# Kernel optimization log

Measured on AMD Instinct MI355X. Metric: run time of the kernel, lower is better.

## Reference

```python
import jax, jax.numpy as jnp
import numpy as np

N_NODES = 50000
N_EDGES = 800000
D_IN = 128
D_OUT = 128
N_GRAPHS = 64
NEG_SLOPE = 0.01  # torch F.leaky_relu default


def gcn_conv(x, W, b, src, dst, n_nodes):
    """PyG GCNConv: linear, add self-loops, symmetric norm, scatter-add, bias."""
    h = x @ W  # [N, D_OUT]
    # degree including self-loop (edge_weight = 1)
    deg = jnp.zeros((n_nodes,), x.dtype).at[dst].add(1.0) + 1.0
    dinv = jax.lax.rsqrt(deg)
    norm = dinv[src] * dinv[dst]           # [E]
    agg = jnp.zeros_like(h).at[dst].add(h[src] * norm[:, None])
    # self-loop contribution: dinv[i]*dinv[i]*h[i] = h[i]/deg[i]
    return agg + h * (1.0 / deg)[:, None] + b


def gcn_branch(x, edge_index, Ws, bs):
    src, dst = edge_index[0], edge_index[1]
    n = x.shape[0]
    for W, b in zip(Ws, bs):
        x = gcn_conv(x, W, b, src, dst, n)
        x = jax.nn.leaky_relu(x, NEG_SLOPE)
        # dropout is identity in eval mode
    return x


def mean_pool(x, batch, num_graphs):
    s = jax.ops.segment_sum(x, batch, num_segments=num_graphs)
    cnt = jax.ops.segment_sum(jnp.ones((x.shape[0],), x.dtype), batch, num_segments=num_graphs)
    return s / jnp.maximum(cnt, 1.0)[:, None]


def setup_inputs() -> dict:
    key = jax.random.key(0)
    ks = jax.random.split(key, 20)
    inp = {
        'x1': jax.random.normal(ks[0], (N_NODES, D_IN), jnp.float32),
        'edge_index1': jax.random.randint(ks[1], (2, N_EDGES), 0, N_NODES, jnp.int64 if jax.config.jax_enable_x64 else jnp.int32),
        'batch1': jnp.sort(jax.random.randint(ks[2], (N_NODES,), 0, N_GRAPHS)),
        'x2': jax.random.normal(ks[3], (N_NODES, D_IN), jnp.float32),
        'edge_index2': jax.random.randint(ks[4], (2, N_EDGES), 0, N_NODES, jnp.int64 if jax.config.jax_enable_x64 else jnp.int32),
        'batch2': jnp.sort(jax.random.randint(ks[5], (N_NODES,), 0, N_GRAPHS)),
    }
    s = 1.0 / np.sqrt(D_IN)
    inp['W1_0'] = jax.random.uniform(ks[6], (D_IN, D_OUT), jnp.float32, -s, s)
    inp['b1_0'] = jnp.zeros((D_OUT,), jnp.float32)
    inp['W1_1'] = jax.random.uniform(ks[7], (D_OUT, D_OUT), jnp.float32, -s, s)
    inp['b1_1'] = jnp.zeros((D_OUT,), jnp.float32)
    inp['W2_0'] = jax.random.uniform(ks[8], (D_IN, D_OUT), jnp.float32, -s, s)
    inp['b2_0'] = jnp.zeros((D_OUT,), jnp.float32)
    inp['W2_1'] = jax.random.uniform(ks[9], (D_OUT, D_OUT), jnp.float32, -s, s)
    inp['b2_1'] = jnp.zeros((D_OUT,), jnp.float32)
    s2 = 1.0 / np.sqrt(2 * D_OUT)
    inp['lin1_W'] = jax.random.uniform(ks[10], (2 * D_OUT, D_OUT), jnp.float32, -s2, s2)
    inp['lin1_b'] = jax.random.uniform(ks[11], (D_OUT,), jnp.float32, -s2, s2)
    s3 = 1.0 / np.sqrt(D_OUT)
    inp['lin2_W'] = jax.random.uniform(ks[12], (D_OUT, 1), jnp.float32, -s3, s3)
    inp['lin2_b'] = jax.random.uniform(ks[13], (1,), jnp.float32, -s3, s3)
    return inp


def reference(x1, edge_index1, batch1, x2, edge_index2, batch2,
              W1_0, b1_0, W1_1, b1_1, W2_0, b2_0, W2_1, b2_1,
              lin1_W, lin1_b, lin2_W, lin2_b):
    h1 = gcn_branch(x1, edge_index1, [W1_0, W1_1], [b1_0, b1_1])
    h1 = mean_pool(h1, batch1, N_GRAPHS)
    h2 = gcn_branch(x2, edge_index2, [W2_0, W2_1], [b2_0, b2_1])
    h2 = mean_pool(h2, batch2, N_GRAPHS)
    h = jnp.concatenate([h1, h2], axis=-1)  # [G, 256]
    h = jax.nn.relu(h @ lin1_W + lin1_b)
    return h @ lin2_W + lin2_b  # [G, 1]
```

## Files before the change

kernel.cpp:

```cpp
#include <hip/hip_runtime.h>
#include <hip/hip_fp16.h>

#define N_NODES 50000
#define N_EDGES 800000
#define D 128
#define N_GRAPHS 64
#define NEG_SLOPE 0.01f
#define ELLW 32
#define OVF_CAP 8192

#define BUCKETS 196
#define NPAD (BUCKETS * 256)
#define EPB 2048
#define BCAP 5120
#define XS 136
#define NR (N_NODES + 16)
#define EMPTY_IDX 50000
#define EMPTY_FILL 0xC350C350u
#define AGG_BLKS (N_NODES / 16)

typedef _Float16 half8 __attribute__((ext_vector_type(8)));
typedef _Float16 half4 __attribute__((ext_vector_type(4)));
typedef float f32x4 __attribute__((ext_vector_type(4)));
typedef float f32x2 __attribute__((ext_vector_type(2)));

__device__ __forceinline__ int lower_bound_i(const int* __restrict__ arr, int n, int key) {
    int lo = 0, hi = n;
    while (lo < hi) {
        int mid = (lo + hi) >> 1;
        if (arr[mid] < key) lo = mid + 1; else hi = mid;
    }
    return lo;
}

__global__ __launch_bounds__(256) void k_prep(const float* __restrict__ Wa, const float* __restrict__ Wb,
                                              const float* __restrict__ Wc, const float* __restrict__ Wd,
                                              const int* __restrict__ batch1, const int* __restrict__ batch2,
                                              __half* __restrict__ WtH, int* __restrict__ gcnt,
                                              float* __restrict__ pp, int* __restrict__ cntg,
                                              unsigned char* __restrict__ H8a, unsigned char* __restrict__ H8b) {
    const float* Ws[4] = {Wa, Wb, Wc, Wd};
    const float* W = Ws[blockIdx.x];
    __half* o = WtH + (size_t)blockIdx.x * 16384;
    int t = threadIdx.x;
    for (int r = 0; r < 64; r++) {
        int e = r * 256 + t;
        int k = e >> 7, n = e & 127;
        o[n * 128 + k] = __float2half(W[k * 128 + n]);
    }
#pragma unroll
    for (int i = 0; i < 16; i++) pp[blockIdx.x * 4096 + i * 256 + t] = 0.0f;
    {
        unsigned char* z = (blockIdx.x < 2 ? H8a : H8b) + (size_t)(blockIdx.x & 1) * NR * 128 + (size_t)N_NODES * 128;
        if (t < 32) ((unsigned int*)z)[t] = 0u;
    }
    if (blockIdx.x == 0) {
        for (int i = t; i < 2 * BUCKETS + 8; i += 256) gcnt[i] = 0;
    }
    if (blockIdx.x == 1) {
        if (t < 64)
            cntg[t] = lower_bound_i(batch1, N_NODES, t + 1) - lower_bound_i(batch1, N_NODES, t);
        else if (t < 128)
            cntg[t] = lower_bound_i(batch2, N_NODES, (t - 64) + 1) - lower_bound_i(batch2, N_NODES, t - 64);
    }
}

__global__ __launch_bounds__(256) void k_part(const int* __restrict__ ei1, const int* __restrict__ ei2,
                                              int* __restrict__ gcnt, int2* __restrict__ bucketed) {
    const int br = blockIdx.x & 1;
    const int blk = blockIdx.x >> 1;
    const int* __restrict__ src = (br ? ei2 : ei1);
    const int* __restrict__ dst = src + N_EDGES;
    int* __restrict__ gc = gcnt + br * BUCKETS;
    int2* __restrict__ bk = bucketed + (size_t)br * BUCKETS * BCAP;

    __shared__ int bcnt[BUCKETS];
    __shared__ int bofs[BUCKETS];
    __shared__ int gbase[BUCKETS];
    __shared__ int sc[BUCKETS];
    __shared__ int stot;
    __shared__ int2 stage[EPB];
    const int tid = threadIdx.x;
    const int base = blk * EPB;
    for (int b = tid; b < BUCKETS; b += 256) bcnt[b] = 0;
    __syncthreads();
    int d_[8], s_[8], p_[8];
#pragma unroll
    for (int k = 0; k < 8; k++) {
        int i = base + k * 256 + tid;
        bool v = i < N_EDGES;
        d_[k] = v ? dst[i] : -1;
        s_[k] = v ? src[i] : 0;
        p_[k] = 0;
        if (v) p_[k] = atomicAdd(&bcnt[d_[k] >> 8], 1);
    }
    __syncthreads();
    if (tid < BUCKETS) sc[tid] = bcnt[tid];
    __syncthreads();
    for (int off = 1; off < BUCKETS; off <<= 1) {
        int v = (tid < BUCKETS && tid >= off) ? sc[tid - off] : 0;
        __syncthreads();
        if (tid < BUCKETS) sc[tid] += v;
        __syncthreads();
    }
    if (tid < BUCKETS) {
        bofs[tid] = sc[tid] - bcnt[tid];
        gbase[tid] = atomicAdd(&gc[tid], bcnt[tid]);
    }
    if (tid == BUCKETS - 1) stot = sc[tid];
    __syncthreads();
#pragma unroll
    for (int k = 0; k < 8; k++) {
        if (d_[k] >= 0) stage[bofs[d_[k] >> 8] + p_[k]] = make_int2(d_[k], s_[k]);
    }
    __syncthreads();
    int total = stot;
    for (int i = tid; i < total; i += 256) {
        int2 e = stage[i];
        int b = e.x >> 8;
        int dest = gbase[b] + (i - bofs[b]);
        if (dest < BCAP) bk[(size_t)b * BCAP + dest] = e;
    }
}

__global__ __launch_bounds__(256) void k_build(const int* __restrict__ gcnt, const int2* __restrict__ bucketed,
                                               int* __restrict__ cnti, unsigned short* __restrict__ ell,
                                               int2* __restrict__ ovf, int* __restrict__ ocnt) {
    const int br = blockIdx.x & 1;
    const int b = blockIdx.x >> 1;
    const int* __restrict__ gc = gcnt + br * BUCKETS;
    const int2* __restrict__ bk = bucketed + (size_t)br * BUCKETS * BCAP;
    int* __restrict__ ci = cnti + br * NPAD;
    unsigned short* __restrict__ el = ell + (size_t)br * NPAD * ELLW;
    int2* __restrict__ ov = ovf + (size_t)br * OVF_CAP;
    int* __restrict__ oc = ocnt + br;

    __shared__ unsigned short lell[256 * ELLW];
    __shared__ int lcnt[256];
    const int tid = threadIdx.x;
    lcnt[tid] = 0;
#pragma unroll
    for (int i = 0; i < 4; i++) ((uint4*)lell)[tid + 256 * i] = make_uint4(EMPTY_FILL, EMPTY_FILL, EMPTY_FILL, EMPTY_FILL);
    __syncthreads();
    int nb = min(gc[b], BCAP);
    const int2* __restrict__ bp = bk + (size_t)b * BCAP;
    for (int i = tid; i < nb; i += 256) {
        int2 e = bp[i];
        int dl = e.x & 255;
        int p = atomicAdd(&lcnt[dl], 1);
        if (p < ELLW) {
            lell[dl * ELLW + p] = (unsigned short)e.y;
        } else {
            int o = atomicAdd(oc, 1);
            if (o < OVF_CAP) ov[o] = e;
        }
    }
    __syncthreads();
    ci[b * 256 + tid] = lcnt[tid];
    uint4* eg = (uint4*)(el + (size_t)b * 256 * ELLW);
    const uint4* elc = (const uint4*)lell;
    for (int i = tid; i < 256 * ELLW * 2 / 16; i += 256) eg[i] = elc[i];
}

template <bool FP16IN>
__global__ __launch_bounds__(256) void k_gemm(const void* __restrict__ xin1, const void* __restrict__ xin2,
                                              const __half* __restrict__ WtHall, int layer,
                                              const int* __restrict__ cnti, unsigned char* __restrict__ H8) {
    const int br = blockIdx.y;
    const void* __restrict__ xin = (br ? xin2 : xin1);
    const __half* __restrict__ WtH = WtHall + (size_t)(br * 2 + layer) * 16384;
    const int* __restrict__ cnt = cnti + br * NPAD;
    unsigned char* __restrict__ h = H8 + (size_t)br * NR * 128;

    __shared__ _Float16 Xl[64 * XS];
    __shared__ _Float16 Wt[128 * XS];
    const int tid = threadIdx.x;
    const int w = tid >> 6, lane = tid & 63;
    const int quad = lane >> 4, l16 = lane & 15;
    const int row0 = blockIdx.x * 64;

#pragma unroll
    for (int i = 0; i < 8; i++) {
        int i2 = tid + 256 * i;
        int r = i2 >> 4, cg = i2 & 15;
        *(uint4*)&Wt[r * XS + cg * 8] = ((const uint4*)WtH)[i2];
    }
    if (FP16IN) {
        const __half* x = (const __half*)xin;
#pragma unroll
        for (int i = 0; i < 4; i++) {
            int i2 = tid + 256 * i;
            int r = i2 >> 4, cg = i2 & 15;
            uint4 v = make_uint4(0, 0, 0, 0);
            if (row0 + r < N_NODES) v = ((const uint4*)(x + (size_t)(row0 + r) * D))[cg];
            *(uint4*)&Xl[r * XS + cg * 8] = v;
        }
    } else {
        const float* x = (const float*)xin;
#pragma unroll
        for (int i = 0; i < 8; i++) {
            int i2 = tid + 256 * i;
            int r = i2 >> 5, f4 = i2 & 31;
            float4 v = make_float4(0.f, 0.f, 0.f, 0.f);
            if (row0 + r < N_NODES) v = *(const float4*)((const float*)x + (size_t)(row0 + r) * D + f4 * 4);
            half4 hv;
            hv[0] = (_Float16)v.x; hv[1] = (_Float16)v.y; hv[2] = (_Float16)v.z; hv[3] = (_Float16)v.w;
            *(half4*)&Xl[r * XS + f4 * 4] = hv;
        }
    }
    __syncthreads();

    half8 a[4];
#pragma unroll
    for (int kb = 0; kb < 4; kb++)
        a[kb] = *(const half8*)&Xl[(w * 16 + l16) * XS + kb * 32 + quad * 8];

    const int rbase = row0 + w * 16 + quad * 4;
    float di[4];
#pragma unroll
    for (int reg = 0; reg < 4; reg++) {
        int r = rbase + reg;
        di[reg] = (r < N_NODES) ? rsqrtf((float)cnt[r] + 1.0f) : 0.0f;
    }

    float accs[8][4];
#pragma unroll
    for (int ct = 0; ct < 8; ct++) {
        f32x4 acc = {0.f, 0.f, 0.f, 0.f};
#pragma unroll
        for (int kb = 0; kb < 4; kb++) {
            half8 b = *(const half8*)&Wt[(ct * 16 + l16) * XS + kb * 32 + quad * 8];
            acc = __builtin_amdgcn_mfma_f32_16x16x32_f16(a[kb], b, acc, 0, 0, 0);
        }
#pragma unroll
        for (int reg = 0; reg < 4; reg++) accs[ct][reg] = acc[reg] * di[reg];
    }

    __syncthreads();
    unsigned char* S = (unsigned char*)Xl;
#pragma unroll
    for (int ct = 0; ct < 8; ct++)
#pragma unroll
        for (int reg = 0; reg < 4; reg++) {
            int p = __builtin_amdgcn_cvt_pk_fp8_f32(accs[ct][reg], accs[ct][reg], 0, false);
            S[(w * 16 + quad * 4 + reg) * 128 + ct * 16 + l16] = (unsigned char)p;
        }
    __syncthreads();
#pragma unroll
    for (int i = 0; i < 2; i++) {
        int idx = tid + 256 * i;
        int r = idx >> 3, cg = idx & 7;
        if (row0 + r < N_NODES)
            ((uint4*)(h + (size_t)(row0 + r) * 128))[cg] = ((const uint4*)S)[idx];
    }
}

#define AGG_ISSUE(buf, g) do {                                                             \
    unsigned int iw0 = *(const unsigned int*)&sidx[nq][(g) * 8 + 0];                       \
    unsigned int iw1 = *(const unsigned int*)&sidx[nq][(g) * 8 + 2];                       \
    unsigned int iw2 = *(const unsigned int*)&sidx[nq][(g) * 8 + 4];                       \
    unsigned int iw3 = *(const unsigned int*)&sidx[nq][(g) * 8 + 6];                       \
    buf[0] = *(const unsigned int*)(H8 + (size_t)(iw0 & 0xffffu) * 128 + hofs + l16 * 4);  \
    buf[1] = *(const unsigned int*)(H8 + (size_t)(iw0 >> 16) * 128 + hofs + l16 * 4);      \
    buf[2] = *(const unsigned int*)(H8 + (size_t)(iw1 & 0xffffu) * 128 + hofs + l16 * 4);  \
    buf[3] = *(const unsigned int*)(H8 + (size_t)(iw1 >> 16) * 128 + hofs + l16 * 4);      \
    buf[4] = *(const unsigned int*)(H8 + (size_t)(iw2 & 0xffffu) * 128 + hofs + l16 * 4);  \
    buf[5] = *(const unsigned int*)(H8 + (size_t)(iw2 >> 16) * 128 + hofs + l16 * 4);      \
    buf[6] = *(const unsigned int*)(H8 + (size_t)(iw3 & 0xffffu) * 128 + hofs + l16 * 4);  \
    buf[7] = *(const unsigned int*)(H8 + (size_t)(iw3 >> 16) * 128 + hofs + l16 * 4);      \
} while (0)

#define AGG_CONSUME(buf) do {                                                              \
    _Pragma("unroll")                                                                      \
    for (int i_ = 0; i_ < 8; i_++) {                                                       \
        f32x2 lo = __builtin_amdgcn_cvt_pk_f32_fp8((int)buf[i_], false);                   \
        f32x2 hi = __builtin_amdgcn_cvt_pk_f32_fp8((int)buf[i_], true);                    \
        accv[i_ & 3].x += lo[0];                                                           \
        accv[i_ & 3].y += lo[1];                                                           \
        accv[i_ & 3].z += hi[0];                                                           \
        accv[i_ & 3].w += hi[1];                                                           \
    }                                                                                      \
} while (0)

#define AGG_CORE()                                                                         \
    float4 accv[4];                                                                        \
    {                                                                                      \
        f32x2 lo = __builtin_amdgcn_cvt_pk_f32_fp8((int)dself, false);                     \
        f32x2 hi = __builtin_amdgcn_cvt_pk_f32_fp8((int)dself, true);                      \
        accv[0] = make_float4(lo[0], lo[1], hi[0], hi[1]);                                 \
    }                                                                                      \
    accv[1] = make_float4(0.f, 0.f, 0.f, 0.f); accv[2] = accv[1]; accv[3] = accv[1];       \
    unsigned int bA_[8], bB_[8], bC_[8], bD_[8];                                           \
    AGG_ISSUE(bA_, 0);                                                                     \
    if (nc > 8)  { AGG_ISSUE(bB_, 1); }                                                    \
    if (nc > 16) { AGG_ISSUE(bC_, 2); }                                                    \
    if (nc > 24) { AGG_ISSUE(bD_, 3); }                                                    \
    AGG_CONSUME(bA_);                                                                      \
    if (nc > 8)  { AGG_CONSUME(bB_); }                                                     \
    if (nc > 16) { AGG_CONSUME(bC_); }                                                     \
    if (nc > 24) { AGG_CONSUME(bD_); }

__global__ __launch_bounds__(256) void k_agg(const int* __restrict__ cnti, const unsigned short* __restrict__ ell,
                                             const int2* __restrict__ ovf, const int* __restrict__ ocnt,
                                             const unsigned char* __restrict__ H8all, const float* __restrict__ bias1,
                                             const float* __restrict__ bias2, __half* __restrict__ ACT) {
    const int tid = threadIdx.x;
    const int l16 = tid & 15;
    const int nq = tid >> 4;
    const int br = blockIdx.x & 1;
    const int rest = blockIdx.x >> 1;
    const int half = rest >= AGG_BLKS ? 1 : 0;
    const int blk = rest - half * AGG_BLKS;
    const int node = blk * 16 + nq;
    const int hofs = half * 64;

    const int* __restrict__ cnt = cnti + br * NPAD;
    const unsigned short* __restrict__ el = ell + (size_t)br * NPAD * ELLW;
    const int2* __restrict__ ov = ovf + (size_t)br * OVF_CAP;
    const unsigned char* __restrict__ H8 = H8all + (size_t)br * NR * 128;
    const float* __restrict__ bias = (br ? bias2 : bias1);
    __half* __restrict__ out = ACT + (size_t)br * N_NODES * D;

    __shared__ unsigned short sidx[16][ELLW];
    if (tid < 64) ((uint4*)sidx)[tid] = ((const uint4*)(el + (size_t)blk * 16 * ELLW))[tid];

    int n = cnt[node];
    int nc = min(n, ELLW);
    unsigned int dself = *(const unsigned int*)(H8 + (size_t)node * 128 + hofs + l16 * 4);
    __syncthreads();

    AGG_CORE();

    if (n > ELLW) {
        int oc = min(ocnt[br], OVF_CAP);
        for (int o = 0; o < oc; o++) {
            int2 p = ov[o];
            if (p.x == node) {
                unsigned int dw = *(const unsigned int*)(H8 + (size_t)p.y * 128 + hofs + l16 * 4);
                f32x2 lo = __builtin_amdgcn_cvt_pk_f32_fp8((int)dw, false);
                f32x2 hi = __builtin_amdgcn_cvt_pk_f32_fp8((int)dw, true);
                accv[0].x += lo[0]; accv[0].y += lo[1]; accv[0].z += hi[0]; accv[0].w += hi[1];
            }
        }
    }
    float sx = (accv[0].x + accv[1].x) + (accv[2].x + accv[3].x);
    float sy = (accv[0].y + accv[1].y) + (accv[2].y + accv[3].y);
    float sz = (accv[0].z + accv[1].z) + (accv[2].z + accv[3].z);
    float sw = (accv[0].w + accv[1].w) + (accv[2].w + accv[3].w);
    float dv = rsqrtf((float)n + 1.0f);
    float4 b = ((const float4*)bias)[half * 16 + l16];
    float vx = sx * dv + b.x;
    float vy = sy * dv + b.y;
    float vz = sz * dv + b.z;
    float vw = sw * dv + b.w;
    vx = vx > 0.0f ? vx : NEG_SLOPE * vx;
    vy = vy > 0.0f ? vy : NEG_SLOPE * vy;
    vz = vz > 0.0f ? vz : NEG_SLOPE * vz;
    vw = vw > 0.0f ? vw : NEG_SLOPE * vw;
    union { __half2 h2[2]; uint2 u; } up;
    up.h2[0] = __floats2half2_rn(vx, vy);
    up.h2[1] = __floats2half2_rn(vz, vw);
    *(uint2*)(out + (size_t)node * 128 + half * 64 + l16 * 4) = up.u;
}

__global__ __launch_bounds__(256) void k_aggpool(const int* __restrict__ cnti, const unsigned short* __restrict__ ell,
                                                 const int2* __restrict__ ovf, const int* __restrict__ ocnt,
                                                 const unsigned char* __restrict__ H8all,
                                                 const float* __restrict__ bias1, const float* __restrict__ bias2,
                                                 const int* __restrict__ batch1, const int* __restrict__ batch2,
                                                 float* __restrict__ ppall) {
    const int tid = threadIdx.x;
    const int l16 = tid & 15;
    const int nq = tid >> 4;
    const int br = blockIdx.x & 1;
    const int rest = blockIdx.x >> 1;
    const int half = rest >= AGG_BLKS ? 1 : 0;
    const int blk = rest - half * AGG_BLKS;
    const int node = blk * 16 + nq;
    const int hofs = half * 64;

    const int* __restrict__ cnt = cnti + br * NPAD;
    const unsigned short* __restrict__ el = ell + (size_t)br * NPAD * ELLW;
    const int2* __restrict__ ov = ovf + (size_t)br * OVF_CAP;
    const unsigned char* __restrict__ H8 = H8all + (size_t)br * NR * 128;
    const float* __restrict__ bias = (br ? bias2 : bias1);
    const int* __restrict__ batch = (br ? batch2 : batch1);
    float* __restrict__ pp = ppall + (size_t)br * N_GRAPHS * D;

    __shared__ unsigned short sidx[16][ELLW];
    if (tid < 64) ((uint4*)sidx)[tid] = ((const uint4*)(el + (size_t)blk * 16 * ELLW))[tid];

    int n = cnt[node];
    int nc = min(n, ELLW);
    unsigned int dself = *(const unsigned int*)(H8 + (size_t)node * 128 + hofs + l16 * 4);
    __syncthreads();

    AGG_CORE();

    if (n > ELLW) {
        int oc = min(ocnt[br], OVF_CAP);
        for (int o = 0; o < oc; o++) {
            int2 p = ov[o];
            if (p.x == node) {
                unsigned int dw = *(const unsigned int*)(H8 + (size_t)p.y * 128 + hofs + l16 * 4);
                f32x2 lo = __builtin_amdgcn_cvt_pk_f32_fp8((int)dw, false);
                f32x2 hi = __builtin_amdgcn_cvt_pk_f32_fp8((int)dw, true);
                accv[0].x += lo[0]; accv[0].y += lo[1]; accv[0].z += hi[0]; accv[0].w += hi[1];
            }
        }
    }
    float sx = (accv[0].x + accv[1].x) + (accv[2].x + accv[3].x);
    float sy = (accv[0].y + accv[1].y) + (accv[2].y + accv[3].y);
    float sz = (accv[0].z + accv[1].z) + (accv[2].z + accv[3].z);
    float sw = (accv[0].w + accv[1].w) + (accv[2].w + accv[3].w);
    float dv = rsqrtf((float)n + 1.0f);
    float4 b = ((const float4*)bias)[half * 16 + l16];
    float vx = sx * dv + b.x;
    float vy = sy * dv + b.y;
    float vz = sz * dv + b.z;
    float vw = sw * dv + b.w;
    vx = vx > 0.0f ? vx : NEG_SLOPE * vx;
    vy = vy > 0.0f ? vy : NEG_SLOPE * vy;
    vz = vz > 0.0f ? vz : NEG_SLOPE * vz;
    vw = vw > 0.0f ? vw : NEG_SLOPE * vw;
    __half2 q0 = __floats2half2_rn(vx, vy);
    __half2 q1 = __floats2half2_rn(vz, vw);
    float2 f0 = __half22float2(q0);
    float2 f1 = __half22float2(q1);

    __shared__ float sacc[16][64];
    __shared__ int sg[16];
    *(float4*)&sacc[nq][l16 * 4] = make_float4(f0.x, f0.y, f1.x, f1.y);
    if (l16 == 0) sg[nq] = batch[node];
    __syncthreads();
    if (tid < 64) {
        float s = sacc[0][tid];
        int g = sg[0];
        for (int r2 = 1; r2 < 16; r2++) {
            if (sg[r2] == g) {
                s += sacc[r2][tid];
            } else {
                atomicAdd(&pp[(size_t)g * D + half * 64 + tid], s);
                s = sacc[r2][tid];
                g = sg[r2];
            }
        }
        atomicAdd(&pp[(size_t)g * D + half * 64 + tid], s);
    }
}

__global__ __launch_bounds__(128) void k_mlp(const float* __restrict__ pp, const int* __restrict__ cntg,
                                             const float* __restrict__ lin1W, const float* __restrict__ lin1b,
                                             const float* __restrict__ lin2W, const float* __restrict__ lin2b,
                                             float* __restrict__ out) {
    int g = blockIdx.x;
    int c = threadIdx.x;
    __shared__ float cat[2 * D];
    cat[c] = pp[(size_t)g * D + c] / fmaxf((float)cntg[g], 1.0f);
    cat[c + D] = pp[(size_t)(N_GRAPHS + g) * D + c] / fmaxf((float)cntg[64 + g], 1.0f);
    __syncthreads();
    float acc = lin1b[c];
#pragma unroll 8
    for (int k = 0; k < 2 * D; k++) acc += cat[k] * lin1W[k * D + c];
    acc = fmaxf(acc, 0.0f);
    float v = acc * lin2W[c];
#pragma unroll
    for (int off = 32; off > 0; off >>= 1) v += __shfl_down(v, off, 64);
    __shared__ float wsum[2];
    if ((c & 63) == 0) wsum[c >> 6] = v;
    __syncthreads();
    if (c == 0) out[g] = wsum[0] + wsum[1] + lin2b[0];
}

extern "C" void kernel_launch(void* const* d_in, const int* in_sizes, int n_in,
                              void* d_out, int out_size, void* d_ws, size_t ws_size,
                              hipStream_t stream) {
    const float* x1 = (const float*)d_in[0];
    const int*   ei1 = (const int*)d_in[1];
    const int*   batch1 = (const int*)d_in[2];
    const float* x2 = (const float*)d_in[3];
    const int*   ei2 = (const int*)d_in[4];
    const int*   batch2 = (const int*)d_in[5];
    const float* W1_0 = (const float*)d_in[6];
    const float* b1_0 = (const float*)d_in[7];
    const float* W1_1 = (const float*)d_in[8];
    const float* b1_1 = (const float*)d_in[9];
    const float* W2_0 = (const float*)d_in[10];
    const float* b2_0 = (const float*)d_in[11];
    const float* W2_1 = (const float*)d_in[12];
    const float* b2_1 = (const float*)d_in[13];
    const float* lin1W = (const float*)d_in[14];
    const float* lin1b = (const float*)d_in[15];
    const float* lin2W = (const float*)d_in[16];
    const float* lin2b = (const float*)d_in[17];
    float* out = (float*)d_out;

    __half* WtH = (__half*)d_ws;
    __half* ACT = WtH + 65536;
    unsigned char* H8a = (unsigned char*)(ACT + 2 * (size_t)N_NODES * D);
    unsigned char* H8b = H8a + 2 * (size_t)NR * 128;
    unsigned short* ell = (unsigned short*)(H8b + 2 * (size_t)NR * 128);
    int2*   bucketed = (int2*)(ell + 2 * (size_t)NPAD * ELLW);
    int*    cnti = (int*)(bucketed + 2 * (size_t)BUCKETS * BCAP);
    int*    gcnt = cnti + 2 * NPAD;
    int*    ocnt = gcnt + 2 * BUCKETS;
    int*    cntg = ocnt + 8;
    int2*   ovf  = (int2*)(cntg + 128);
    float*  pp   = (float*)(ovf + 2 * (size_t)OVF_CAP);

    dim3 b256(256);
    int partBlocks = (N_EDGES + EPB - 1) / EPB;
    int gemmBlocks = (N_NODES + 63) / 64;
    int aggGrid    = AGG_BLKS * 4;

    k_prep<<<4, b256, 0, stream>>>(W1_0, W1_1, W2_0, W2_1, batch1, batch2, WtH, gcnt, pp, cntg, H8a, H8b);

    k_part  <<<partBlocks * 2, b256, 0, stream>>>(ei1, ei2, gcnt, bucketed);
    k_build <<<BUCKETS * 2,    b256, 0, stream>>>(gcnt, bucketed, cnti, ell, ovf, ocnt);

    k_gemm<false><<<dim3(gemmBlocks, 2), b256, 0, stream>>>(x1, x2, WtH, 0, cnti, H8a);
    k_agg        <<<aggGrid,             b256, 0, stream>>>(cnti, ell, ovf, ocnt, H8a, b1_0, b2_0, ACT);
    k_gemm<true> <<<dim3(gemmBlocks, 2), b256, 0, stream>>>(ACT, ACT + (size_t)N_NODES * D, WtH, 1, cnti, H8b);
    k_aggpool    <<<aggGrid,             b256, 0, stream>>>(cnti, ell, ovf, ocnt, H8b, b1_1, b2_1, batch1, batch2, pp);

    k_mlp<<<N_GRAPHS, dim3(128), 0, stream>>>(pp, cntg, lin1W, lin1b, lin2W, lin2b, out);
}
```

Measured before the change: 280.6 us.

## Build ELL adjacency directly with global atomics instead of bucketed two-pass partition

```diff
diff --git a/kernel.cpp b/kernel.cpp
--- a/kernel.cpp
+++ b/kernel.cpp
@@ -9,10 +9,8 @@
 #define ELLW 32
 #define OVF_CAP 8192
 
-#define BUCKETS 196
-#define NPAD (BUCKETS * 256)
+#define NPAD 50176
 #define EPB 2048
-#define BCAP 5120
 #define XS 136
 #define NR (N_NODES + 16)
 #define EMPTY_IDX 50000
@@ -36,130 +34,67 @@
 __global__ __launch_bounds__(256) void k_prep(const float* __restrict__ Wa, const float* __restrict__ Wb,
                                               const float* __restrict__ Wc, const float* __restrict__ Wd,
                                               const int* __restrict__ batch1, const int* __restrict__ batch2,
-                                              __half* __restrict__ WtH, int* __restrict__ gcnt,
+                                              __half* __restrict__ WtH, int* __restrict__ cnti,
+                                              unsigned short* __restrict__ ell,
                                               float* __restrict__ pp, int* __restrict__ cntg,
                                               unsigned char* __restrict__ H8a, unsigned char* __restrict__ H8b) {
-    const float* Ws[4] = {Wa, Wb, Wc, Wd};
-    const float* W = Ws[blockIdx.x];
-    __half* o = WtH + (size_t)blockIdx.x * 16384;
-    int t = threadIdx.x;
-    for (int r = 0; r < 64; r++) {
-        int e = r * 256 + t;
-        int k = e >> 7, n = e & 127;
-        o[n * 128 + k] = __float2half(W[k * 128 + n]);
-    }
-#pragma unroll
-    for (int i = 0; i < 16; i++) pp[blockIdx.x * 4096 + i * 256 + t] = 0.0f;
-    {
-        unsigned char* z = (blockIdx.x < 2 ? H8a : H8b) + (size_t)(blockIdx.x & 1) * NR * 128 + (size_t)N_NODES * 128;
+    const int b = blockIdx.x;
+    const int t = threadIdx.x;
+    if (b < 4) {
+        const float* Ws[4] = {Wa, Wb, Wc, Wd};
+        const float* W = Ws[b];
+        __half* o = WtH + (size_t)b * 16384;
+        for (int r = 0; r < 64; r++) {
+            int e = r * 256 + t;
+            int k = e >> 7, n = e & 127;
+            o[n * 128 + k] = __float2half(W[k * 128 + n]);
+        }
+#pragma unroll
+        for (int i = 0; i < 16; i++) pp[b * 4096 + i * 256 + t] = 0.0f;
+        unsigned char* z = (b < 2 ? H8a : H8b) + (size_t)(b & 1) * NR * 128 + (size_t)N_NODES * 128;
         if (t < 32) ((unsigned int*)z)[t] = 0u;
-    }
-    if (blockIdx.x == 0) {
-        for (int i = t; i < 2 * BUCKETS + 8; i += 256) gcnt[i] = 0;
-    }
-    if (blockIdx.x == 1) {
-        if (t < 64)
-            cntg[t] = lower_bound_i(batch1, N_NODES, t + 1) - lower_bound_i(batch1, N_NODES, t);
-        else if (t < 128)
-            cntg[t] = lower_bound_i(batch2, N_NODES, (t - 64) + 1) - lower_bound_i(batch2, N_NODES, t - 64);
-    }
-}
-
-__global__ __launch_bounds__(256) void k_part(const int* __restrict__ ei1, const int* __restrict__ ei2,
-                                              int* __restrict__ gcnt, int2* __restrict__ bucketed) {
+        if (b == 1) {
+            if (t < 64)
+                cntg[t] = lower_bound_i(batch1, N_NODES, t + 1) - lower_bound_i(batch1, N_NODES, t);
+            else if (t < 128)
+                cntg[t] = lower_bound_i(batch2, N_NODES, (t - 64) + 1) - lower_bound_i(batch2, N_NODES, t - 64);
+        }
+    } else if (b < 104) {
+        uint4* e4 = (uint4*)ell;
+        const uint4 f = make_uint4(EMPTY_FILL, EMPTY_FILL, EMPTY_FILL, EMPTY_FILL);
+        for (int i = (b - 4) * 256 + t; i < 2 * NPAD * ELLW / 8; i += 100 * 256) e4[i] = f;
+    } else {
+        for (int i = (b - 104) * 256 + t; i < 2 * NPAD + 8; i += 16 * 256) cnti[i] = 0;
+    }
+}
+
+__global__ __launch_bounds__(256) void k_ell(const int* __restrict__ ei1, const int* __restrict__ ei2,
+                                             int* __restrict__ cnti, unsigned short* __restrict__ ell,
+                                             int2* __restrict__ ovf, int* __restrict__ ocnt) {
     const int br = blockIdx.x & 1;
     const int blk = blockIdx.x >> 1;
     const int* __restrict__ src = (br ? ei2 : ei1);
     const int* __restrict__ dst = src + N_EDGES;
-    int* __restrict__ gc = gcnt + br * BUCKETS;
-    int2* __restrict__ bk = bucketed + (size_t)br * BUCKETS * BCAP;
-
-    __shared__ int bcnt[BUCKETS];
-    __shared__ int bofs[BUCKETS];
-    __shared__ int gbase[BUCKETS];
-    __shared__ int sc[BUCKETS];
-    __shared__ int stot;
-    __shared__ int2 stage[EPB];
-    const int tid = threadIdx.x;
-    const int base = blk * EPB;
-    for (int b = tid; b < BUCKETS; b += 256) bcnt[b] = 0;
-    __syncthreads();
-    int d_[8], s_[8], p_[8];
-#pragma unroll
-    for (int k = 0; k < 8; k++) {
-        int i = base + k * 256 + tid;
-        bool v = i < N_EDGES;
-        d_[k] = v ? dst[i] : -1;
-        s_[k] = v ? src[i] : 0;
-        p_[k] = 0;
-        if (v) p_[k] = atomicAdd(&bcnt[d_[k] >> 8], 1);
-    }
-    __syncthreads();
-    if (tid < BUCKETS) sc[tid] = bcnt[tid];
-    __syncthreads();
-    for (int off = 1; off < BUCKETS; off <<= 1) {
-        int v = (tid < BUCKETS && tid >= off) ? sc[tid - off] : 0;
-        __syncthreads();
-        if (tid < BUCKETS) sc[tid] += v;
-        __syncthreads();
-    }
-    if (tid < BUCKETS) {
-        bofs[tid] = sc[tid] - bcnt[tid];
-        gbase[tid] = atomicAdd(&gc[tid], bcnt[tid]);
-    }
-    if (tid == BUCKETS - 1) stot = sc[tid];
-    __syncthreads();
-#pragma unroll
-    for (int k = 0; k < 8; k++) {
-        if (d_[k] >= 0) stage[bofs[d_[k] >> 8] + p_[k]] = make_int2(d_[k], s_[k]);
-    }
-    __syncthreads();
-    int total = stot;
-    for (int i = tid; i < total; i += 256) {
-        int2 e = stage[i];
-        int b = e.x >> 8;
-        int dest = gbase[b] + (i - bofs[b]);
-        if (dest < BCAP) bk[(size_t)b * BCAP + dest] = e;
-    }
-}
-
-__global__ __launch_bounds__(256) void k_build(const int* __restrict__ gcnt, const int2* __restrict__ bucketed,
-                                               int* __restrict__ cnti, unsigned short* __restrict__ ell,
-                                               int2* __restrict__ ovf, int* __restrict__ ocnt) {
-    const int br = blockIdx.x & 1;
-    const int b = blockIdx.x >> 1;
-    const int* __restrict__ gc = gcnt + br * BUCKETS;
-    const int2* __restrict__ bk = bucketed + (size_t)br * BUCKETS * BCAP;
-    int* __restrict__ ci = cnti + br * NPAD;
+    int* __restrict__ cnt = cnti + br * NPAD;
     unsigned short* __restrict__ el = ell + (size_t)br * NPAD * ELLW;
     int2* __restrict__ ov = ovf + (size_t)br * OVF_CAP;
     int* __restrict__ oc = ocnt + br;
 
-    __shared__ unsigned short lell[256 * ELLW];
-    __shared__ int lcnt[256];
-    const int tid = threadIdx.x;
-    lcnt[tid] = 0;
-#pragma unroll
-    for (int i = 0; i < 4; i++) ((uint4*)lell)[tid + 256 * i] = make_uint4(EMPTY_FILL, EMPTY_FILL, EMPTY_FILL, EMPTY_FILL);
-    __syncthreads();
-    int nb = min(gc[b], BCAP);
-    const int2* __restrict__ bp = bk + (size_t)b * BCAP;
-    for (int i = tid; i < nb; i += 256) {
-        int2 e = bp[i];
-        int dl = e.x & 255;
-        int p = atomicAdd(&lcnt[dl], 1);
-        if (p < ELLW) {
-            lell[dl * ELLW + p] = (unsigned short)e.y;
-        } else {
-            int o = atomicAdd(oc, 1);
-            if (o < OVF_CAP) ov[o] = e;
-        }
-    }
-    __syncthreads();
-    ci[b * 256 + tid] = lcnt[tid];
-    uint4* eg = (uint4*)(el + (size_t)b * 256 * ELLW);
-    const uint4* elc = (const uint4*)lell;
-    for (int i = tid; i < 256 * ELLW * 2 / 16; i += 256) eg[i] = elc[i];
+    const int base = blk * EPB + threadIdx.x;
+#pragma unroll
+    for (int k = 0; k < 8; k++) {
+        int i = base + k * 256;
+        if (i < N_EDGES) {
+            int d = dst[i], s = src[i];
+            int p = atomicAdd(&cnt[d], 1);
+            if (p < ELLW) {
+                el[(size_t)d * ELLW + p] = (unsigned short)s;
+            } else {
+                int o = atomicAdd(oc, 1);
+                if (o < OVF_CAP) ov[o] = make_int2(d, s);
+            }
+        }
+    }
 }
 
 template <bool FP16IN>
@@ -500,23 +435,20 @@
     unsigned char* H8a = (unsigned char*)(ACT + 2 * (size_t)N_NODES * D);
     unsigned char* H8b = H8a + 2 * (size_t)NR * 128;
     unsigned short* ell = (unsigned short*)(H8b + 2 * (size_t)NR * 128);
-    int2*   bucketed = (int2*)(ell + 2 * (size_t)NPAD * ELLW);
-    int*    cnti = (int*)(bucketed + 2 * (size_t)BUCKETS * BCAP);
-    int*    gcnt = cnti + 2 * NPAD;
-    int*    ocnt = gcnt + 2 * BUCKETS;
+    int*    cnti = (int*)(ell + 2 * (size_t)NPAD * ELLW);
+    int*    ocnt = cnti + 2 * NPAD;
     int*    cntg = ocnt + 8;
     int2*   ovf  = (int2*)(cntg + 128);
     float*  pp   = (float*)(ovf + 2 * (size_t)OVF_CAP);
 
     dim3 b256(256);
-    int partBlocks = (N_EDGES + EPB - 1) / EPB;
+    int ellBlocks  = (N_EDGES + EPB - 1) / EPB;
     int gemmBlocks = (N_NODES + 63) / 64;
     int aggGrid    = AGG_BLKS * 4;
 
-    k_prep<<<4, b256, 0, stream>>>(W1_0, W1_1, W2_0, W2_1, batch1, batch2, WtH, gcnt, pp, cntg, H8a, H8b);
-
-    k_part  <<<partBlocks * 2, b256, 0, stream>>>(ei1, ei2, gcnt, bucketed);
-    k_build <<<BUCKETS * 2,    b256, 0, stream>>>(gcnt, bucketed, cnti, ell, ovf, ocnt);
+    k_prep<<<120, b256, 0, stream>>>(W1_0, W1_1, W2_0, W2_1, batch1, batch2, WtH, cnti, ell, pp, cntg, H8a, H8b);
+
+    k_ell<<<ellBlocks * 2, b256, 0, stream>>>(ei1, ei2, cnti, ell, ovf, ocnt);
 
     k_gemm<false><<<dim3(gemmBlocks, 2), b256, 0, stream>>>(x1, x2, WtH, 0, cnti, H8a);
     k_agg        <<<aggGrid,             b256, 0, stream>>>(cnti, ell, ovf, ocnt, H8a, b1_0, b2_0, ACT);
```

After: 382.0 us. 1.36x slower.
